# Performance work log

Measured on AMD Instinct MI355X. Metric: run time of the kernel, lower is better.

Reference implementation:

```python
import jax, jax.numpy as jnp
import numpy as np

M, N, K = 4096, 8192, 4096


def setup_inputs() -> dict:
    key = jax.random.key(0)
    k1, k2, k3, k4 = jax.random.split(key, 4)
    a = jax.random.randint(k1, (M, K), 0, 127, dtype=jnp.int32)  # int8 activations
    b = jax.random.randint(k2, (N, K), 0, 127, dtype=jnp.int32)  # int8 weights (row-major [N,K])
    alpha_row = jax.random.uniform(k3, (M, 1), dtype=jnp.float16)  # per-row dequant scale
    alpha_col = jax.random.uniform(k4, (1, N), dtype=jnp.float16)  # per-col dequant scale
    return {"a": a, "b": b, "alpha_row": alpha_row, "alpha_col": alpha_col}


def reference(a, b, alpha_row, alpha_col):
    # x = a @ b.T in fp32 (int8 values upcast), then rescale by outer product of scales
    x = jnp.matmul(a.astype(jnp.float32), b.astype(jnp.float32).T)  # [M, N]
    scale = alpha_row.astype(jnp.float32) * alpha_col.astype(jnp.float32)  # [M, N] via broadcast
    out = x * scale
    return out.astype(jnp.float16)
```

## Files before the change

### kernel.cpp

```cpp
#include <hip/hip_runtime.h>
#include <cstdint>
#include <cstddef>

#define M_DIM 4096
#define N_DIM 8192
#define K_DIM 4096

typedef __attribute__((ext_vector_type(4))) int int4v;

__global__ void __launch_bounds__(256) pack_kernel(const int* __restrict__ a,
                                                   const int* __restrict__ b,
                                                   unsigned char* __restrict__ pa,
                                                   unsigned char* __restrict__ pb) {
    size_t t = (size_t)blockIdx.x * 256 + threadIdx.x;
    const size_t NA16 = (size_t)M_DIM * K_DIM / 16;
    const int* __restrict__ src;
    unsigned char* __restrict__ dst;
    if (t < NA16) {
        src = a; dst = pa;
    } else {
        src = b; dst = pb; t -= NA16;
    }
    const int4v* s4 = (const int4v*)src + t * 4;
    int4v o;
#pragma unroll
    for (int q = 0; q < 4; ++q) {
        int4v v = s4[q];
        o[q] = (v[0] & 0xff) | ((v[1] & 0xff) << 8) | ((v[2] & 0xff) << 16) | (v[3] << 24);
    }
    ((int4v*)dst)[t] = o;
}

__device__ inline void async_copy16(const unsigned char* g, unsigned char* l) {
    __builtin_amdgcn_global_load_lds(
        (const __attribute__((address_space(1))) void*)g,
        (__attribute__((address_space(3))) void*)l,
        16, 0, 0);
}

__global__ void __launch_bounds__(256) gemm_i8(const unsigned char* __restrict__ Ap,
                                               const unsigned char* __restrict__ Bp,
                                               const _Float16* __restrict__ arow,
                                               const _Float16* __restrict__ acol,
                                               _Float16* __restrict__ Cout) {
    __shared__ __align__(16) unsigned char As[128 * 128];
    __shared__ __align__(16) unsigned char Bs[128 * 128];

    const int tid  = threadIdx.x;
    const int lane = tid & 63;
    const int wave = tid >> 6;
    const int bn   = blockIdx.x;
    const int bm   = blockIdx.y;

    const int wm = (wave & 1) * 64;
    const int wn = (wave >> 1) * 64;

    const size_t a_row0 = (size_t)bm * 128;
    const size_t b_row0 = (size_t)bn * 128;

    const int srow   = lane >> 3;
    const int schunk = (lane & 7) ^ srow;
    const unsigned char* ag = Ap + (a_row0 + wave * 32 + srow) * (size_t)K_DIM + schunk * 16;
    const unsigned char* bg = Bp + (b_row0 + wave * 32 + srow) * (size_t)K_DIM + schunk * 16;
    unsigned char* al = As + wave * 4096;
    unsigned char* bl = Bs + wave * 4096;

    const int fr_x0    = (((lane >> 4) ^ (lane & 7)) << 4);
    const int a_fr_row = wm + (lane & 15);
    const int b_fr_row = wn + (lane & 15);

    int4v acc[4][4];
#pragma unroll
    for (int i = 0; i < 4; ++i)
#pragma unroll
        for (int j = 0; j < 4; ++j) acc[i][j] = (int4v)0;

    for (int kt = 0; kt < K_DIM; kt += 128) {
#pragma unroll
        for (int r4 = 0; r4 < 4; ++r4) {
            async_copy16(ag + kt + r4 * 8 * K_DIM, al + r4 * 1024);
            async_copy16(bg + kt + r4 * 8 * K_DIM, bl + r4 * 1024);
        }
        __syncthreads();

#pragma unroll
        for (int h = 0; h < 2; ++h) {
            const int off = fr_x0 ^ (h << 6);
            int4v af[4], bf[4];
#pragma unroll
            for (int i = 0; i < 4; ++i)
                af[i] = *(const int4v*)(As + (size_t)(a_fr_row + i * 16) * 128 + off);
#pragma unroll
            for (int j = 0; j < 4; ++j)
                bf[j] = *(const int4v*)(Bs + (size_t)(b_fr_row + j * 16) * 128 + off);

#pragma unroll
            for (int i = 0; i < 4; ++i)
#pragma unroll
                for (int j = 0; j < 4; ++j)
                    acc[i][j] = __builtin_amdgcn_mfma_i32_16x16x64_i8(af[i], bf[j],
                                                                      acc[i][j], 0, 0, 0);
        }
        __syncthreads();
    }

    const int gcol0 = (int)b_row0 + wn + (lane & 15);
    float ac4[4];
#pragma unroll
    for (int j = 0; j < 4; ++j) ac4[j] = (float)acol[gcol0 + j * 16];

    const size_t grow0 = a_row0 + wm + (lane >> 4) * 4;
#pragma unroll
    for (int i = 0; i < 4; ++i) {
#pragma unroll
        for (int r = 0; r < 4; ++r) {
            const size_t row = grow0 + i * 16 + r;
            const float ar = (float)arow[row];
            _Float16* outp = Cout + row * (size_t)N_DIM + gcol0;
#pragma unroll
            for (int j = 0; j < 4; ++j) {
                float v = (float)acc[i][j][r] * ar * ac4[j];
                outp[j * 16] = (_Float16)v;
            }
        }
    }
}

extern "C" void kernel_launch(void* const* d_in, const int* in_sizes, int n_in,
                              void* d_out, int out_size, void* d_ws, size_t ws_size,
                              hipStream_t stream) {
    const int* a = (const int*)d_in[0];
    const int* b = (const int*)d_in[1];
    const _Float16* ar = (const _Float16*)d_in[2];
    const _Float16* ac = (const _Float16*)d_in[3];
    _Float16* out = (_Float16*)d_out;

    unsigned char* pa = (unsigned char*)d_ws;
    unsigned char* pb = pa + (size_t)M_DIM * K_DIM;

    const int pack_blocks = (int)(((size_t)M_DIM * K_DIM + (size_t)N_DIM * K_DIM) / 16 / 256);
    pack_kernel<<<pack_blocks, 256, 0, stream>>>(a, b, pa, pb);

    dim3 grid(N_DIM / 128, M_DIM / 128);
    gemm_i8<<<grid, 256, 0, stream>>>(pa, pb, ar, ac, out);
}
```

Measured before the change: 393.0 us.

## Pack int8 operands in MFMA fragment order and load A directly to registers

The pack kernel now writes A and B in MFMA fragment-major order (16-row panels, 64-byte k-slices, per-lane 16-byte chunks) instead of plain row-major int8. The GEMM kernel loads A fragments straight from global memory into registers with coalesced 16-byte-per-lane reads, which removes the A shared-memory tile and its LDS traffic. B is still staged through LDS with async copies, now contiguous so no XOR swizzle is needed. The trade-off is that A rows are fetched by each wave with no sharing through LDS, and the global loads sit on the critical path before the barrier without prefetching.

Measured after the change: 392.8 us. No clear change (-0.1%).

```diff
diff --git a/kernel.cpp b/kernel.cpp
--- a/kernel.cpp
+++ b/kernel.cpp
@@ -8,24 +8,28 @@
 
 typedef __attribute__((ext_vector_type(4))) int int4v;
 
-__global__ void __launch_bounds__(256) pack_kernel(const int* __restrict__ a,
-                                                   const int* __restrict__ b,
-                                                   unsigned char* __restrict__ pa,
-                                                   unsigned char* __restrict__ pb) {
+__global__ void __launch_bounds__(256) pack_frag(const int* __restrict__ a,
+                                                 const int* __restrict__ b,
+                                                 unsigned char* __restrict__ pa,
+                                                 unsigned char* __restrict__ pb) {
     size_t t = (size_t)blockIdx.x * 256 + threadIdx.x;
-    const size_t NA16 = (size_t)M_DIM * K_DIM / 16;
+    const size_t NA = (size_t)(M_DIM / 16) * (K_DIM / 64) * 64;
     const int* __restrict__ src;
     unsigned char* __restrict__ dst;
-    if (t < NA16) {
+    if (t < NA) {
         src = a; dst = pa;
     } else {
-        src = b; dst = pb; t -= NA16;
+        src = b; dst = pb; t -= NA;
     }
-    const int4v* s4 = (const int4v*)src + t * 4;
+    const int l = (int)(t & 63);
+    const int s = (int)((t >> 6) & 63);
+    const int p = (int)(t >> 12);
+    const int* g = src + ((size_t)(16 * p + (l & 15))) * K_DIM + s * 64 + (l >> 4) * 16;
+    const int4v* g4 = (const int4v*)g;
     int4v o;
 #pragma unroll
     for (int q = 0; q < 4; ++q) {
-        int4v v = s4[q];
+        int4v v = g4[q];
         o[q] = (v[0] & 0xff) | ((v[1] & 0xff) << 8) | ((v[2] & 0xff) << 16) | (v[3] << 24);
     }
     ((int4v*)dst)[t] = o;
@@ -43,8 +47,7 @@
                                                const _Float16* __restrict__ arow,
                                                const _Float16* __restrict__ acol,
                                                _Float16* __restrict__ Cout) {
-    __shared__ __align__(16) unsigned char As[128 * 128];
-    __shared__ __align__(16) unsigned char Bs[128 * 128];
+    __shared__ __align__(16) unsigned char Bs[16384];
 
     const int tid  = threadIdx.x;
     const int lane = tid & 63;
@@ -55,19 +58,20 @@
     const int wm = (wave & 1) * 64;
     const int wn = (wave >> 1) * 64;
 
-    const size_t a_row0 = (size_t)bm * 128;
-    const size_t b_row0 = (size_t)bn * 128;
+    const unsigned char* Abase =
+        Ap + ((size_t)(bm * 8 + (wm >> 4))) * 65536 + lane * 16;
 
-    const int srow   = lane >> 3;
-    const int schunk = (lane & 7) ^ srow;
-    const unsigned char* ag = Ap + (a_row0 + wave * 32 + srow) * (size_t)K_DIM + schunk * 16;
-    const unsigned char* bg = Bp + (b_row0 + wave * 32 + srow) * (size_t)K_DIM + schunk * 16;
-    unsigned char* al = As + wave * 4096;
-    unsigned char* bl = Bs + wave * 4096;
+    const size_t Bblk = (size_t)bn * 8 * 65536;
+    const unsigned char* bg[4];
+    unsigned char* bl[4];
+#pragma unroll
+    for (int r = 0; r < 4; ++r) {
+        const int offu = r * 4096 + wave * 1024;
+        bg[r] = Bp + Bblk + (size_t)(offu >> 11) * 65536 + (offu & 2047) + lane * 16;
+        bl[r] = Bs + offu;
+    }
 
-    const int fr_x0    = (((lane >> 4) ^ (lane & 7)) << 4);
-    const int a_fr_row = wm + (lane & 15);
-    const int b_fr_row = wn + (lane & 15);
+    const int bf_base = ((wn >> 4) << 11) + lane * 16;
 
     int4v acc[4][4];
 #pragma unroll
@@ -75,41 +79,42 @@
 #pragma unroll
         for (int j = 0; j < 4; ++j) acc[i][j] = (int4v)0;
 
-    for (int kt = 0; kt < K_DIM; kt += 128) {
+    for (int T = 0; T < K_DIM / 128; ++T) {
+        const int gk = T * 2048;
+
+        int4v af[2][4];
 #pragma unroll
-        for (int r4 = 0; r4 < 4; ++r4) {
-            async_copy16(ag + kt + r4 * 8 * K_DIM, al + r4 * 1024);
-            async_copy16(bg + kt + r4 * 8 * K_DIM, bl + r4 * 1024);
-        }
+        for (int h = 0; h < 2; ++h)
+#pragma unroll
+            for (int i = 0; i < 4; ++i)
+                af[h][i] = *(const int4v*)(Abase + (size_t)i * 65536 + gk + h * 1024);
+
+#pragma unroll
+        for (int r = 0; r < 4; ++r) async_copy16(bg[r] + gk, bl[r]);
         __syncthreads();
 
 #pragma unroll
         for (int h = 0; h < 2; ++h) {
-            const int off = fr_x0 ^ (h << 6);
-            int4v af[4], bf[4];
-#pragma unroll
-            for (int i = 0; i < 4; ++i)
-                af[i] = *(const int4v*)(As + (size_t)(a_fr_row + i * 16) * 128 + off);
+            int4v bf[4];
 #pragma unroll
             for (int j = 0; j < 4; ++j)
-                bf[j] = *(const int4v*)(Bs + (size_t)(b_fr_row + j * 16) * 128 + off);
-
+                bf[j] = *(const int4v*)(Bs + bf_base + j * 2048 + h * 1024);
 #pragma unroll
             for (int i = 0; i < 4; ++i)
 #pragma unroll
                 for (int j = 0; j < 4; ++j)
-                    acc[i][j] = __builtin_amdgcn_mfma_i32_16x16x64_i8(af[i], bf[j],
+                    acc[i][j] = __builtin_amdgcn_mfma_i32_16x16x64_i8(af[h][i], bf[j],
                                                                       acc[i][j], 0, 0, 0);
         }
         __syncthreads();
     }
 
-    const int gcol0 = (int)b_row0 + wn + (lane & 15);
+    const int gcol0 = bn * 128 + wn + (lane & 15);
     float ac4[4];
 #pragma unroll
     for (int j = 0; j < 4; ++j) ac4[j] = (float)acol[gcol0 + j * 16];
 
-    const size_t grow0 = a_row0 + wm + (lane >> 4) * 4;
+    const size_t grow0 = (size_t)bm * 128 + wm + (lane >> 4) * 4;
 #pragma unroll
     for (int i = 0; i < 4; ++i) {
 #pragma unroll
@@ -138,8 +143,8 @@
     unsigned char* pa = (unsigned char*)d_ws;
     unsigned char* pb = pa + (size_t)M_DIM * K_DIM;
 
-    const int pack_blocks = (int)(((size_t)M_DIM * K_DIM + (size_t)N_DIM * K_DIM) / 16 / 256);
-    pack_kernel<<<pack_blocks, 256, 0, stream>>>(a, b, pa, pb);
+    const size_t total_frag = (size_t)(M_DIM / 16 + N_DIM / 16) * (K_DIM / 64) * 64;
+    pack_frag<<<(int)(total_frag / 256), 256, 0, stream>>>(a, b, pa, pb);
 
     dim3 grid(N_DIM / 128, M_DIM / 128);
     gemm_i8<<<grid, 256, 0, stream>>>(pa, pb, ar, ac, out);
```
